# Kernel optimization log

Hardware: AMD Instinct MI355X
Metric: run time of the kernel (lower is better)

The kernel has to match this reference:

```python
import jax, jax.numpy as jnp
import numpy as np
import math

E = 4096  # embed_dim
H = 32    # num_heads
M = 256   # max_queries
B = 8     # batch
N = 256   # kv tokens (16x16 grid -> no pos-embed interpolation branch)


def _sincos_1d(d, pos):
    omega = np.arange(d // 2, dtype=np.float32) / (d / 2.0)
    omega = 1.0 / 10000 ** omega
    out = np.einsum('m,d->md', pos.reshape(-1), omega)
    return np.concatenate([np.sin(out), np.cos(out)], axis=1)


def _sincos_2d(embed_dim, grid_size):
    gh = np.arange(grid_size, dtype=np.float32)
    gw = np.arange(grid_size, dtype=np.float32)
    grid = np.stack(np.meshgrid(gw, gh), axis=0).reshape(2, -1)
    return np.concatenate([
        _sincos_1d(embed_dim // 2, grid[0]),
        _sincos_1d(embed_dim // 2, grid[1]),
    ], axis=1)


def setup_inputs() -> dict:
    key = jax.random.key(0)
    ks = jax.random.split(key, 4)
    grid_size = int(math.ceil(math.sqrt(M)))
    pe = _sincos_2d(E, grid_size)[:M].astype(np.float32)
    return {
        'x': jax.random.normal(ks[0], (B, N, E), jnp.float32),
        'query': 0.02 * jax.random.normal(ks[1], (M, E), jnp.float32),
        'pos_embed': jnp.asarray(pe),
        'ln_q_w': jnp.ones((E,), jnp.float32),
        'ln_q_b': jnp.zeros((E,), jnp.float32),
        'ln_kv_w': jnp.ones((E,), jnp.float32),
        'ln_kv_b': jnp.zeros((E,), jnp.float32),
        'in_proj_w': 0.02 * jax.random.normal(ks[2], (3 * E, E), jnp.float32),
        'in_proj_b': jnp.zeros((3 * E,), jnp.float32),
        'out_proj_w': 0.02 * jax.random.normal(ks[3], (E, E), jnp.float32),
        'out_proj_b': jnp.zeros((E,), jnp.float32),
    }


def _ln(x, w, b, eps=1e-5):
    m = jnp.mean(x, -1, keepdims=True)
    v = jnp.mean((x - m) ** 2, -1, keepdims=True)
    return (x - m) * jax.lax.rsqrt(v + eps) * w + b


def reference(x, query, pos_embed, ln_q_w, ln_q_b, ln_kv_w, ln_kv_b,
              in_proj_w, in_proj_b, out_proj_w, out_proj_b):
    D = E // H
    kv = _ln(x, ln_kv_w, ln_kv_b)                      # [B,N,E] (kv_proj is Identity)
    q_in = _ln(query, ln_q_w, ln_q_b) + pos_embed      # [M,E] (Q + posQ, shared over batch)
    k_in = kv + pos_embed[None]                        # N == M so posK == pos_embed (no interp)
    Wq, Wk, Wv = in_proj_w[:E], in_proj_w[E:2 * E], in_proj_w[2 * E:]
    bq, bk, bv = in_proj_b[:E], in_proj_b[E:2 * E], in_proj_b[2 * E:]
    q = (q_in @ Wq.T + bq).reshape(M, H, D).transpose(1, 0, 2)          # [H,M,D]
    k = (k_in @ Wk.T + bk).reshape(B, N, H, D).transpose(0, 2, 1, 3)    # [B,H,N,D]
    v = (kv @ Wv.T + bv).reshape(B, N, H, D).transpose(0, 2, 1, 3)      # [B,H,N,D]
    scores = jnp.einsum('hmd,bhnd->bhmn', q, k) / jnp.sqrt(jnp.float32(D))
    attn = jax.nn.softmax(scores, axis=-1)                              # [B,H,M,N]
    o = jnp.einsum('bhmn,bhnd->bhmd', attn, v)
    o = o.transpose(0, 2, 1, 3).reshape(B, M, E)
    out = o @ out_proj_w.T + out_proj_b                                 # [B,M,E]
    # need_weights=True with average_attn_weights=True -> head-averaged weights
    return out, attn.mean(axis=1)
```

## Files before the change

kernel.cpp:

```cpp
#include <hip/hip_runtime.h>
#include <hip/hip_bf16.h>

typedef __bf16 bf16;
typedef __attribute__((ext_vector_type(8))) __bf16 bf16x8;
typedef __attribute__((ext_vector_type(4))) __bf16 bf16x4;
typedef __attribute__((ext_vector_type(4))) float floatx4;

#define E_DIM 4096
#define H_DIM 32
#define D_DIM 128
#define M_DIM 256
#define B_DIM 8
#define N_DIM 256

#define GLD_LDS(g, l) __builtin_amdgcn_global_load_lds( \
    (const __attribute__((address_space(1))) unsigned int*)(g), \
    (__attribute__((address_space(3))) unsigned int*)(l), 16, 0, 0)

__device__ __forceinline__ float wave_sum(float v) {
#pragma unroll
  for (int o = 32; o; o >>= 1) v += __shfl_xor(v, o);
  return v;
}
__device__ __forceinline__ float wave_max(float v) {
#pragma unroll
  for (int o = 32; o; o >>= 1) v = fmaxf(v, __shfl_xor(v, o));
  return v;
}

__device__ __forceinline__ void gemm_core(const bf16* __restrict__ Arow,
                                          const bf16* __restrict__ Brow,
                                          int lda, int ldb, int kTiles,
                                          bf16* As, bf16* Bs,
                                          floatx4 (&acc)[4][4],
                                          int wid, int lane) {
  const int s0 = wid * 2;
  const int lp = lane ^ ((lane >> 3) & 7);
  const int srow = lp >> 2;
  const int skoff = (lp & 3) * 8;
  const int rA = (wid >> 1) * 64 + (lane & 15);
  const int rB = (wid & 1) * 64 + (lane & 15);
  const int q16 = (lane >> 4) * 8;
  const int ex = (((lane & 15) >> 1) & 7) << 3;

#pragma unroll
  for (int c = 0; c < 2; ++c) {
    const int s = s0 + c;
    const int row = s * 16 + srow;
    GLD_LDS(Arow + (size_t)row * lda + skoff, As + s * 512);
    GLD_LDS(Brow + (size_t)row * ldb + skoff, Bs + s * 512);
  }

  for (int kt = 0; kt < kTiles; ++kt) {
    const int cur = (kt & 1) * 4096;
    const int nxt = 4096 - cur;
    __syncthreads();
    if (kt + 1 < kTiles) {
      const int k0 = (kt + 1) << 5;
#pragma unroll
      for (int c = 0; c < 2; ++c) {
        const int s = s0 + c;
        const int row = s * 16 + srow;
        GLD_LDS(Arow + (size_t)row * lda + k0 + skoff, As + nxt + s * 512);
        GLD_LDS(Brow + (size_t)row * ldb + k0 + skoff, Bs + nxt + s * 512);
      }
    }
    bf16x8 af[4], bfr[4];
#pragma unroll
    for (int t = 0; t < 4; ++t) {
      af[t] = *(const bf16x8*)(As + cur + ((((rA + t * 16) * 32) + q16) ^ ex));
      bfr[t] = *(const bf16x8*)(Bs + cur + ((((rB + t * 16) * 32) + q16) ^ ex));
    }
#pragma unroll
    for (int tr = 0; tr < 4; ++tr)
#pragma unroll
      for (int tc = 0; tc < 4; ++tc)
        acc[tr][tc] = __builtin_amdgcn_mfma_f32_16x16x32_bf16(af[tr], bfr[tc],
                                                              acc[tr][tc], 0, 0, 0);
  }
}

__global__ __launch_bounds__(256) void cvt_all_kernel(const float* __restrict__ s1,
                                                      bf16* __restrict__ d1,
                                                      const float* __restrict__ s2,
                                                      bf16* __restrict__ d2) {
  long i = ((long)blockIdx.x * 256 + threadIdx.x) * 8;
  const float* src;
  bf16* dst;
  if (i < 50331648L) { src = s1 + i; dst = d1 + i; }
  else { src = s2 + (i - 50331648L); dst = d2 + (i - 50331648L); }
  float4 a = *(const float4*)(src);
  float4 b = *(const float4*)(src + 4);
  bf16x8 p;
  p[0] = (bf16)a.x; p[1] = (bf16)a.y; p[2] = (bf16)a.z; p[3] = (bf16)a.w;
  p[4] = (bf16)b.x; p[5] = (bf16)b.y; p[6] = (bf16)b.z; p[7] = (bf16)b.w;
  *(bf16x8*)(dst) = p;
}

__global__ __launch_bounds__(256) void ln_x_kernel(const float* __restrict__ x,
                                                   const float* __restrict__ w,
                                                   const float* __restrict__ bvec,
                                                   const float* __restrict__ pos,
                                                   bf16* __restrict__ kv,
                                                   bf16* __restrict__ kin) {
  const int row = blockIdx.x;
  const int n = row & (N_DIM - 1);
  const int tid = threadIdx.x, wid = tid >> 6, lane = tid & 63;
  const float* xr = x + (size_t)row * E_DIM;
  float4 v[4];
  float s1 = 0.f, s2 = 0.f;
#pragma unroll
  for (int j = 0; j < 4; ++j) {
    v[j] = *(const float4*)(xr + j * 1024 + tid * 4);
    s1 += v[j].x + v[j].y + v[j].z + v[j].w;
    s2 += v[j].x * v[j].x + v[j].y * v[j].y + v[j].z * v[j].z + v[j].w * v[j].w;
  }
  s1 = wave_sum(s1); s2 = wave_sum(s2);
  __shared__ float red[8];
  if (lane == 0) { red[wid] = s1; red[wid + 4] = s2; }
  __syncthreads();
  s1 = red[0] + red[1] + red[2] + red[3];
  s2 = red[4] + red[5] + red[6] + red[7];
  const float mean = s1 * (1.f / E_DIM);
  const float var = s2 * (1.f / E_DIM) - mean * mean;
  const float rs = rsqrtf(var + 1e-5f);
#pragma unroll
  for (int j = 0; j < 4; ++j) {
    const int idx = j * 1024 + tid * 4;
    float4 wv = *(const float4*)(w + idx);
    float4 bv = *(const float4*)(bvec + idx);
    float4 pv = *(const float4*)(pos + (size_t)n * E_DIM + idx);
    float y0 = (v[j].x - mean) * rs * wv.x + bv.x;
    float y1 = (v[j].y - mean) * rs * wv.y + bv.y;
    float y2 = (v[j].z - mean) * rs * wv.z + bv.z;
    float y3 = (v[j].w - mean) * rs * wv.w + bv.w;
    bf16x4 a; a[0] = (bf16)y0; a[1] = (bf16)y1; a[2] = (bf16)y2; a[3] = (bf16)y3;
    *(bf16x4*)(kv + (size_t)row * E_DIM + idx) = a;
    bf16x4 c; c[0] = (bf16)(y0 + pv.x); c[1] = (bf16)(y1 + pv.y);
    c[2] = (bf16)(y2 + pv.z); c[3] = (bf16)(y3 + pv.w);
    *(bf16x4*)(kin + (size_t)row * E_DIM + idx) = c;
  }
}

__global__ __launch_bounds__(256) void ln_q_kernel(const float* __restrict__ q,
                                                   const float* __restrict__ w,
                                                   const float* __restrict__ bvec,
                                                   const float* __restrict__ pos,
                                                   bf16* __restrict__ qin) {
  const int row = blockIdx.x;
  const int tid = threadIdx.x, wid = tid >> 6, lane = tid & 63;
  const float* xr = q + (size_t)row * E_DIM;
  float4 v[4];
  float s1 = 0.f, s2 = 0.f;
#pragma unroll
  for (int j = 0; j < 4; ++j) {
    v[j] = *(const float4*)(xr + j * 1024 + tid * 4);
    s1 += v[j].x + v[j].y + v[j].z + v[j].w;
    s2 += v[j].x * v[j].x + v[j].y * v[j].y + v[j].z * v[j].z + v[j].w * v[j].w;
  }
  s1 = wave_sum(s1); s2 = wave_sum(s2);
  __shared__ float red[8];
  if (lane == 0) { red[wid] = s1; red[wid + 4] = s2; }
  __syncthreads();
  s1 = red[0] + red[1] + red[2] + red[3];
  s2 = red[4] + red[5] + red[6] + red[7];
  const float mean = s1 * (1.f / E_DIM);
  const float var = s2 * (1.f / E_DIM) - mean * mean;
  const float rs = rsqrtf(var + 1e-5f);
#pragma unroll
  for (int j = 0; j < 4; ++j) {
    const int idx = j * 1024 + tid * 4;
    float4 wv = *(const float4*)(w + idx);
    float4 bv = *(const float4*)(bvec + idx);
    float4 pv = *(const float4*)(pos + (size_t)row * E_DIM + idx);
    bf16x4 a;
    a[0] = (bf16)((v[j].x - mean) * rs * wv.x + bv.x + pv.x);
    a[1] = (bf16)((v[j].y - mean) * rs * wv.y + bv.y + pv.y);
    a[2] = (bf16)((v[j].z - mean) * rs * wv.z + bv.z + pv.z);
    a[3] = (bf16)((v[j].w - mean) * rs * wv.w + bv.w + pv.w);
    *(bf16x4*)(qin + (size_t)row * E_DIM + idx) = a;
  }
}

__global__ __launch_bounds__(256, 4)
void proj_fused(const bf16* __restrict__ qin, const bf16* __restrict__ kin,
                const bf16* __restrict__ kv, const bf16* __restrict__ Wqkv,
                const float* __restrict__ bqkv, bf16* __restrict__ qp,
                bf16* __restrict__ kp, bf16* __restrict__ vt) {
  __shared__ __align__(16) bf16 As[8192];
  __shared__ __align__(16) bf16 Bs[8192];
  const int tid = threadIdx.x;
  const int wid = tid >> 6;
  const int lane = tid & 63;

  const int id = blockIdx.x;
  int role, bx, by;
  const bf16 *A, *B;
  const float* bias;
  bf16* C;
  if (id < 512) {
    role = 1; bx = id & 31; by = id >> 5;
    A = kin; B = Wqkv + 16777216; bias = bqkv + 4096; C = kp;
  } else if (id < 1024) {
    role = 2; bx = (id - 512) & 31; by = (id - 512) >> 5;
    A = kv; B = Wqkv + 33554432; bias = bqkv + 8192; C = vt;
  } else {
    role = 0; bx = (id - 1024) & 31; by = (id - 1024) >> 5;
    A = qin; B = Wqkv; bias = bqkv; C = qp;
  }

  const bf16* Arow = A + (size_t)(by * 128) * E_DIM;
  const bf16* Brow = B + (size_t)(bx * 128) * E_DIM;

  floatx4 acc[4][4];
#pragma unroll
  for (int i = 0; i < 4; ++i)
#pragma unroll
    for (int j = 0; j < 4; ++j) acc[i][j] = (floatx4){0.f, 0.f, 0.f, 0.f};

  gemm_core(Arow, Brow, E_DIM, E_DIM, 128, As, Bs, acc, wid, lane);

  const int mb = by * 128 + (wid >> 1) * 64 + (lane >> 4) * 4;
  const int nb = bx * 128 + (wid & 1) * 64 + (lane & 15);
#pragma unroll
  for (int tr = 0; tr < 4; ++tr) {
#pragma unroll
    for (int tc = 0; tc < 4; ++tc) {
      const int row0 = mb + tr * 16;
      const int col = nb + tc * 16;
      const float bb = bias[col];
      floatx4 a = acc[tr][tc];
      if (role != 2) {
#pragma unroll
        for (int r = 0; r < 4; ++r)
          C[(size_t)(row0 + r) * E_DIM + col] = (bf16)(a[r] + bb);
      } else {
        const int h = col >> 7, d = col & 127;
        const int b_ = row0 >> 8, n_ = row0 & 255;
        bf16x4 p;
#pragma unroll
        for (int r = 0; r < 4; ++r) p[r] = (bf16)(a[r] + bb);
        *(bf16x4*)(C + ((size_t)((b_ * H_DIM + h) * D_DIM + d)) * N_DIM + n_) = p;
      }
    }
  }
}

template <int MODE>
__global__ __launch_bounds__(256, 4)
void gemm_bt(const bf16* __restrict__ Abase, const bf16* __restrict__ Bbase,
             float* __restrict__ Cf, bf16* __restrict__ Cb,
             int K, int lda, int ldb, int ldc, float scale) {
  __shared__ __align__(16) bf16 As[8192];
  __shared__ __align__(16) bf16 Bs[8192];
  const int tid = threadIdx.x;
  const int wid = tid >> 6;
  const int lane = tid & 63;

  const bf16* A = Abase;
  const bf16* B = Bbase;
  if constexpr (MODE == 2) {
    int z = blockIdx.z; int zb = z >> 5, zh = z & 31;
    A += zh * D_DIM;
    B += ((size_t)zb * N_DIM) * E_DIM + zh * D_DIM;
  } else if constexpr (MODE == 3) {
    int z = blockIdx.z;
    A += (size_t)z * M_DIM * 512;
    B += (size_t)z * D_DIM * N_DIM;
  } else if constexpr (MODE == 5) {
    A += blockIdx.z * 2048;
    B += blockIdx.z * 2048;
  }

  const bf16* Arow = A + (size_t)(blockIdx.y * 128) * lda;
  const bf16* Brow = B + (size_t)(blockIdx.x * 128) * ldb;

  floatx4 acc[4][4];
#pragma unroll
  for (int i = 0; i < 4; ++i)
#pragma unroll
    for (int j = 0; j < 4; ++j) acc[i][j] = (floatx4){0.f, 0.f, 0.f, 0.f};

  gemm_core(Arow, Brow, lda, ldb, K >> 5, As, Bs, acc, wid, lane);

  const int mb = blockIdx.y * 128 + (wid >> 1) * 64 + (lane >> 4) * 4;
  const int nb = blockIdx.x * 128 + (wid & 1) * 64 + (lane & 15);
#pragma unroll
  for (int tr = 0; tr < 4; ++tr) {
#pragma unroll
    for (int tc = 0; tc < 4; ++tc) {
      const int row0 = mb + tr * 16;
      const int col = nb + tc * 16;
      floatx4 a = acc[tr][tc];
      if constexpr (MODE == 2) {
#pragma unroll
        for (int r = 0; r < 4; ++r)
          Cf[(size_t)blockIdx.z * (M_DIM * N_DIM) + (size_t)(row0 + r) * ldc + col] =
              a[r] * scale;
      } else if constexpr (MODE == 3) {
        int z = blockIdx.z; int zb_ = z >> 5, zh_ = z & 31;
#pragma unroll
        for (int r = 0; r < 4; ++r)
          Cb[(size_t)zb_ * M_DIM * E_DIM + (size_t)(row0 + r) * E_DIM + zh_ * D_DIM + col] =
              (bf16)a[r];
      } else {
#pragma unroll
        for (int r = 0; r < 4; ++r)
          Cf[(size_t)blockIdx.z * 8388608 + (size_t)(row0 + r) * ldc + col] = a[r];
      }
    }
  }
}

__global__ __launch_bounds__(256) void reduce_out_kernel(const float* __restrict__ p,
                                                         const float* __restrict__ bias,
                                                         float* __restrict__ out) {
  const size_t i = ((size_t)blockIdx.x * 256 + threadIdx.x) * 4;
  float4 a = *(const float4*)(p + i);
  float4 b = *(const float4*)(p + 8388608 + i);
  float4 bb = *(const float4*)(bias + (i & 4095));
  float4 o;
  o.x = a.x + b.x + bb.x; o.y = a.y + b.y + bb.y;
  o.z = a.z + b.z + bb.z; o.w = a.w + b.w + bb.w;
  *(float4*)(out + i) = o;
}

__global__ __launch_bounds__(256) void softmax_mean_kernel(float* __restrict__ scores,
                                                           float* __restrict__ out_mean) {
  const int bm = blockIdx.x;
  const int b = bm >> 8, m = bm & 255;
  const int wid = threadIdx.x >> 6, lane = threadIdx.x & 63;
  float a0 = 0.f, a1 = 0.f, a2 = 0.f, a3 = 0.f;
  for (int j = 0; j < 8; ++j) {
    const int h = wid * 8 + j;
    float* row = scores + ((size_t)((b * H_DIM + h) * M_DIM + m)) * N_DIM;
    float4 v = *(const float4*)(row + lane * 4);
    float mx = fmaxf(fmaxf(v.x, v.y), fmaxf(v.z, v.w));
    mx = wave_max(mx);
    v.x = __expf(v.x - mx); v.y = __expf(v.y - mx);
    v.z = __expf(v.z - mx); v.w = __expf(v.w - mx);
    const float s = wave_sum(v.x + v.y + v.z + v.w);
    const float inv = 1.f / s;
    v.x *= inv; v.y *= inv; v.z *= inv; v.w *= inv;
    a0 += v.x; a1 += v.y; a2 += v.z; a3 += v.w;
    bf16x4 p; p[0] = (bf16)v.x; p[1] = (bf16)v.y; p[2] = (bf16)v.z; p[3] = (bf16)v.w;
    *(bf16x4*)((bf16*)row + lane * 4) = p;
  }
  __shared__ float red[4][256];
  *(float4*)&red[wid][lane * 4] = make_float4(a0, a1, a2, a3);
  __syncthreads();
  if (wid == 0) {
    float4 r0 = *(float4*)&red[0][lane * 4];
    float4 r1 = *(float4*)&red[1][lane * 4];
    float4 r2 = *(float4*)&red[2][lane * 4];
    float4 r3 = *(float4*)&red[3][lane * 4];
    float4 o;
    o.x = (r0.x + r1.x + r2.x + r3.x) * (1.f / H_DIM);
    o.y = (r0.y + r1.y + r2.y + r3.y) * (1.f / H_DIM);
    o.z = (r0.z + r1.z + r2.z + r3.z) * (1.f / H_DIM);
    o.w = (r0.w + r1.w + r2.w + r3.w) * (1.f / H_DIM);
    *(float4*)(out_mean + (size_t)bm * N_DIM + lane * 4) = o;
  }
}

extern "C" void kernel_launch(void* const* d_in, const int* in_sizes, int n_in,
                              void* d_out, int out_size, void* d_ws, size_t ws_size,
                              hipStream_t stream) {
  const float* x = (const float*)d_in[0];
  const float* query = (const float*)d_in[1];
  const float* pos = (const float*)d_in[2];
  const float* ln_q_w = (const float*)d_in[3];
  const float* ln_q_b = (const float*)d_in[4];
  const float* ln_kv_w = (const float*)d_in[5];
  const float* ln_kv_b = (const float*)d_in[6];
  const float* Wqkv_f = (const float*)d_in[7];
  const float* bqkv = (const float*)d_in[8];
  const float* Wout_f = (const float*)d_in[9];
  const float* bout = (const float*)d_in[10];

  char* ws = (char*)d_ws;
  bf16* Wqkv = (bf16*)(ws + 0);
  bf16* Wout = (bf16*)(ws + 100663296);
  bf16* kv   = (bf16*)(ws + 134217728);
  bf16* kin  = (bf16*)(ws + 150994944);
  bf16* qin  = (bf16*)(ws + 167772160);
  bf16* qp   = (bf16*)(ws + 169869312);
  bf16* kp   = (bf16*)(ws + 171966464);
  bf16* vt   = (bf16*)(ws + 188743680);
  float* partials = (float*)(ws + 205520896);
  float* scores = (float*)(ws + 0);
  bf16* obuf = (bf16*)(ws + 67108864);

  float* out = (float*)d_out;
  float* out2 = out + (size_t)B_DIM * M_DIM * E_DIM;

  cvt_all_kernel<<<32768, 256, 0, stream>>>(Wqkv_f, Wqkv, Wout_f, Wout);
  ln_x_kernel<<<2048, 256, 0, stream>>>(x, ln_kv_w, ln_kv_b, pos, kv, kin);
  ln_q_kernel<<<256, 256, 0, stream>>>(query, ln_q_w, ln_q_b, pos, qin);

  proj_fused<<<1088, 256, 0, stream>>>(qin, kin, kv, Wqkv, bqkv, qp, kp, vt);

  gemm_bt<2><<<dim3(2, 2, 256), 256, 0, stream>>>(qp, kp, scores, nullptr,
                                                  128, 4096, 4096, 256,
                                                  0.08838834764831845f);
  softmax_mean_kernel<<<2048, 256, 0, stream>>>(scores, out2);
  gemm_bt<3><<<dim3(1, 2, 256), 256, 0, stream>>>((const bf16*)scores, vt,
                                                  nullptr, obuf,
                                                  256, 512, 256, 4096, 1.f);
  gemm_bt<5><<<dim3(32, 16, 2), 256, 0, stream>>>(obuf, Wout, partials, nullptr,
                                                  2048, 4096, 4096, 4096, 1.f);
  reduce_out_kernel<<<8192, 256, 0, stream>>>(partials, bout, out);
}
```

Baseline: 789.2 us.

## Use 256x256-tile 8-wave pipelined GEMM for QKV and output projections

Replaces the 128x128-tile projection GEMMs with a new 256x256-tile kernel using 512 threads and double-buffered LDS staging via global_load_lds. The main loop interleaves MFMA quarters with async loads, using explicit barriers and setprio. Blocks are remapped in XCD-aware order so the 8 chiplets share the A/B tiles. The larger tiles raise arithmetic intensity and cut global traffic for the two large GEMMs, but give fewer blocks (272 and 256 on 256 CUs) and one block per CU. The small attention GEMMs drop to launch bound 2.

```diff
diff --git a/kernel.cpp b/kernel.cpp
--- a/kernel.cpp
+++ b/kernel.cpp
@@ -28,12 +28,216 @@
   return v;
 }
 
-__device__ __forceinline__ void gemm_core(const bf16* __restrict__ Arow,
-                                          const bf16* __restrict__ Brow,
-                                          int lda, int ldb, int kTiles,
-                                          bf16* As, bf16* Bs,
-                                          floatx4 (&acc)[4][4],
-                                          int wid, int lane) {
+#define BAR256() asm volatile("s_barrier" ::: "memory")
+#define LGKM0_256()                                      \
+  asm volatile("s_waitcnt lgkmcnt(0)" ::: "memory");     \
+  __builtin_amdgcn_sched_barrier(0)
+
+#define STAGE_A256(T, h)                                                       \
+  {                                                                            \
+    _Pragma("unroll") for (int j = 0; j < 2; ++j)                              \
+        GLD_LDS(Ag + (size_t)((h)*128 + sgrow + j * 8) * lda + (T) * 64 + sgcol, \
+                AsP + ((T)&1) * 16384 + (h)*8192 + sdst + j * 512);            \
+  }
+#define STAGE_B256(T, h)                                                       \
+  {                                                                            \
+    _Pragma("unroll") for (int j = 0; j < 2; ++j)                              \
+        GLD_LDS(Bg + (size_t)((h)*128 + sgrow + j * 8) * ldb + (T) * 64 + sgcol, \
+                BsP + ((T)&1) * 16384 + (h)*8192 + sdst + j * 512);            \
+  }
+#define LDA256(mh)                                                             \
+  {                                                                            \
+    _Pragma("unroll") for (int m = 0; m < 4; ++m) {                            \
+      a[m][0] = *(const bf16x8*)(AsP + buf + rA + ((mh)*4 + m) * 1024 + slot0); \
+      a[m][1] = *(const bf16x8*)(AsP + buf + rA + ((mh)*4 + m) * 1024 + slot1); \
+    }                                                                          \
+  }
+#define LDB256(dst, nh)                                                        \
+  {                                                                            \
+    _Pragma("unroll") for (int n = 0; n < 2; ++n) {                            \
+      dst[n][0] = *(const bf16x8*)(BsP + buf + rB + ((nh)*2 + n) * 1024 + slot0); \
+      dst[n][1] = *(const bf16x8*)(BsP + buf + rB + ((nh)*2 + n) * 1024 + slot1); \
+    }                                                                          \
+  }
+#define MFMAQ(mb, nb, B)                                                       \
+  {                                                                            \
+    _Pragma("unroll") for (int m = 0; m < 4; ++m)                              \
+        _Pragma("unroll") for (int n = 0; n < 2; ++n) {                        \
+      acc[(mb) + m][(nb) + n] = __builtin_amdgcn_mfma_f32_16x16x32_bf16(       \
+          a[m][0], B[n][0], acc[(mb) + m][(nb) + n], 0, 0, 0);                 \
+      acc[(mb) + m][(nb) + n] = __builtin_amdgcn_mfma_f32_16x16x32_bf16(       \
+          a[m][1], B[n][1], acc[(mb) + m][(nb) + n], 0, 0, 0);                 \
+    }                                                                          \
+  }
+
+__device__ __forceinline__ void gemm256_core(const bf16* __restrict__ Ag,
+                                             const bf16* __restrict__ Bg,
+                                             int lda, int ldb, int nkt,
+                                             bf16* AsP, bf16* BsP,
+                                             floatx4 (&acc)[8][4],
+                                             int wid, int lane) {
+  const int wm = wid >> 2, wn = wid & 3;
+  const int l15 = lane & 15, q = lane >> 4, e7 = lane & 7;
+  const int slot0 = ((q ^ e7) & 7) * 8;
+  const int slot1 = (((4 + q) ^ e7) & 7) * 8;
+  const int rA = (wm * 128 + l15) * 64;
+  const int rB = (wn * 64 + l15) * 64;
+  const int sgrow = wid * 16 + (lane >> 3);
+  const int sgcol = ((lane & 7) ^ (lane >> 3)) * 8;
+  const int sdst = wid * 1024;
+
+  bf16x8 a[4][2], b0[2][2], b1[2][2];
+
+  STAGE_B256(0, 0); STAGE_B256(0, 1);
+  STAGE_A256(0, 0); STAGE_A256(0, 1);
+  STAGE_B256(1, 0); STAGE_B256(1, 1);
+
+  for (int U = 0; U < nkt; ++U) {
+    const int buf = (U & 1) * 16384;
+    if (U + 1 < nkt)
+      asm volatile("s_waitcnt vmcnt(4)\n\ts_barrier" ::: "memory");
+    else
+      asm volatile("s_waitcnt vmcnt(0)\n\ts_barrier" ::: "memory");
+    LDA256(0); LDB256(b0, 0);
+    if (U + 1 < nkt) { STAGE_A256(U + 1, 0); }
+    BAR256(); LGKM0_256();
+    __builtin_amdgcn_s_setprio(1); MFMAQ(0, 0, b0); __builtin_amdgcn_s_setprio(0);
+    __builtin_amdgcn_sched_barrier(0); BAR256();
+    LDB256(b1, 1);
+    if (U + 1 < nkt) { STAGE_A256(U + 1, 1); }
+    BAR256(); LGKM0_256();
+    __builtin_amdgcn_s_setprio(1); MFMAQ(0, 2, b1); __builtin_amdgcn_s_setprio(0);
+    __builtin_amdgcn_sched_barrier(0); BAR256();
+    LDA256(1);
+    if (U + 2 < nkt) { STAGE_B256(U + 2, 0); }
+    BAR256(); LGKM0_256();
+    __builtin_amdgcn_s_setprio(1); MFMAQ(4, 2, b1); __builtin_amdgcn_s_setprio(0);
+    __builtin_amdgcn_sched_barrier(0); BAR256();
+    if (U + 2 < nkt) { STAGE_B256(U + 2, 1); }
+    BAR256();
+    __builtin_amdgcn_s_setprio(1); MFMAQ(4, 0, b0); __builtin_amdgcn_s_setprio(0);
+    __builtin_amdgcn_sched_barrier(0);
+  }
+}
+
+__global__ __launch_bounds__(512, 1)
+void proj256(const bf16* __restrict__ qin, const bf16* __restrict__ kin,
+             const bf16* __restrict__ kv, const bf16* __restrict__ Wqkv,
+             const float* __restrict__ bqkv, bf16* __restrict__ qp,
+             bf16* __restrict__ kp, bf16* __restrict__ vt) {
+  __shared__ __align__(16) bf16 As2[32768];
+  __shared__ __align__(16) bf16 Bs2[32768];
+  const int tid = threadIdx.x, wid = tid >> 6, lane = tid & 63;
+
+  const int o = blockIdx.x;
+  const int id = (o & 7) * 34 + (o >> 3);
+  int role, bx, by;
+  const bf16 *A, *B;
+  const float* bias;
+  bf16* C;
+  if (id < 128) {
+    role = 1; by = id & 7; bx = id >> 3;
+    A = kin; B = Wqkv + 16777216; bias = bqkv + 4096; C = kp;
+  } else if (id < 256) {
+    role = 2; by = (id - 128) & 7; bx = (id - 128) >> 3;
+    A = kv; B = Wqkv + 33554432; bias = bqkv + 8192; C = vt;
+  } else {
+    role = 0; by = 0; bx = id - 256;
+    A = qin; B = Wqkv; bias = bqkv; C = qp;
+  }
+  const int trowA = by * 256, trowB = bx * 256;
+  const bf16* Ag = A + (size_t)trowA * E_DIM;
+  const bf16* Bg = B + (size_t)trowB * E_DIM;
+
+  floatx4 acc[8][4];
+#pragma unroll
+  for (int i = 0; i < 8; ++i)
+#pragma unroll
+    for (int j = 0; j < 4; ++j) acc[i][j] = (floatx4){0.f, 0.f, 0.f, 0.f};
+
+  gemm256_core(Ag, Bg, E_DIM, E_DIM, 64, As2, Bs2, acc, wid, lane);
+
+  const int wm = wid >> 2, wn = wid & 3;
+  const int l15 = lane & 15, q = lane >> 4;
+  const int mrow0 = trowA + wm * 128 + q * 4;
+  const int ncol0 = trowB + wn * 64 + l15;
+  if (role != 2) {
+#pragma unroll
+    for (int m = 0; m < 8; ++m)
+#pragma unroll
+      for (int n = 0; n < 4; ++n) {
+        const int col = ncol0 + n * 16;
+        const float bb = bias[col];
+        floatx4 v = acc[m][n];
+#pragma unroll
+        for (int r = 0; r < 4; ++r)
+          C[(size_t)(mrow0 + m * 16 + r) * E_DIM + col] = (bf16)(v[r] + bb);
+      }
+  } else {
+#pragma unroll
+    for (int m = 0; m < 8; ++m)
+#pragma unroll
+      for (int n = 0; n < 4; ++n) {
+        const int col = ncol0 + n * 16;
+        const int h = col >> 7, d = col & 127;
+        const float bb = bias[col];
+        const int row0 = mrow0 + m * 16;
+        const int b_ = row0 >> 8, n_ = row0 & 255;
+        floatx4 v = acc[m][n];
+        bf16x4 p;
+#pragma unroll
+        for (int r = 0; r < 4; ++r) p[r] = (bf16)(v[r] + bb);
+        *(bf16x4*)(C + ((size_t)((b_ * H_DIM + h) * D_DIM + d)) * N_DIM + n_) = p;
+      }
+  }
+}
+
+__global__ __launch_bounds__(512, 1)
+void outproj256(const bf16* __restrict__ obuf, const bf16* __restrict__ Wout,
+                float* __restrict__ Cf) {
+  __shared__ __align__(16) bf16 As2[32768];
+  __shared__ __align__(16) bf16 Bs2[32768];
+  const int tid = threadIdx.x, wid = tid >> 6, lane = tid & 63;
+
+  const int o = blockIdx.x;
+  const int id = (o & 7) * 32 + (o >> 3);
+  const int z = id >> 7;
+  const int t = id & 127;
+  const int by = t & 7, bx = t >> 3;
+  const int trowA = by * 256, trowB = bx * 256;
+  const bf16* Ag = obuf + (size_t)z * 2048 + (size_t)trowA * E_DIM;
+  const bf16* Bg = Wout + (size_t)z * 2048 + (size_t)trowB * E_DIM;
+
+  floatx4 acc[8][4];
+#pragma unroll
+  for (int i = 0; i < 8; ++i)
+#pragma unroll
+    for (int j = 0; j < 4; ++j) acc[i][j] = (floatx4){0.f, 0.f, 0.f, 0.f};
+
+  gemm256_core(Ag, Bg, E_DIM, E_DIM, 32, As2, Bs2, acc, wid, lane);
+
+  const int wm = wid >> 2, wn = wid & 3;
+  const int l15 = lane & 15, q = lane >> 4;
+  const int mrow0 = trowA + wm * 128 + q * 4;
+  const int ncol0 = trowB + wn * 64 + l15;
+#pragma unroll
+  for (int m = 0; m < 8; ++m)
+#pragma unroll
+    for (int n = 0; n < 4; ++n) {
+      const int col = ncol0 + n * 16;
+      floatx4 v = acc[m][n];
+#pragma unroll
+      for (int r = 0; r < 4; ++r)
+        Cf[(size_t)z * 8388608 + (size_t)(mrow0 + m * 16 + r) * E_DIM + col] = v[r];
+    }
+}
+
+__device__ __forceinline__ void gemm_core_small(const bf16* __restrict__ Arow,
+                                                const bf16* __restrict__ Brow,
+                                                int lda, int ldb, int kTiles,
+                                                bf16* As, bf16* Bs,
+                                                floatx4 (&acc)[4][4],
+                                                int wid, int lane) {
   const int s0 = wid * 2;
   const int lp = lane ^ ((lane >> 3) & 7);
   const int srow = lp >> 2;
@@ -182,72 +386,8 @@
   }
 }
 
-__global__ __launch_bounds__(256, 4)
-void proj_fused(const bf16* __restrict__ qin, const bf16* __restrict__ kin,
-                const bf16* __restrict__ kv, const bf16* __restrict__ Wqkv,
-                const float* __restrict__ bqkv, bf16* __restrict__ qp,
-                bf16* __restrict__ kp, bf16* __restrict__ vt) {
-  __shared__ __align__(16) bf16 As[8192];
-  __shared__ __align__(16) bf16 Bs[8192];
-  const int tid = threadIdx.x;
-  const int wid = tid >> 6;
-  const int lane = tid & 63;
-
-  const int id = blockIdx.x;
-  int role, bx, by;
-  const bf16 *A, *B;
-  const float* bias;
-  bf16* C;
-  if (id < 512) {
-    role = 1; bx = id & 31; by = id >> 5;
-    A = kin; B = Wqkv + 16777216; bias = bqkv + 4096; C = kp;
-  } else if (id < 1024) {
-    role = 2; bx = (id - 512) & 31; by = (id - 512) >> 5;
-    A = kv; B = Wqkv + 33554432; bias = bqkv + 8192; C = vt;
-  } else {
-    role = 0; bx = (id - 1024) & 31; by = (id - 1024) >> 5;
-    A = qin; B = Wqkv; bias = bqkv; C = qp;
-  }
-
-  const bf16* Arow = A + (size_t)(by * 128) * E_DIM;
-  const bf16* Brow = B + (size_t)(bx * 128) * E_DIM;
-
-  floatx4 acc[4][4];
-#pragma unroll
-  for (int i = 0; i < 4; ++i)
-#pragma unroll
-    for (int j = 0; j < 4; ++j) acc[i][j] = (floatx4){0.f, 0.f, 0.f, 0.f};
-
-  gemm_core(Arow, Brow, E_DIM, E_DIM, 128, As, Bs, acc, wid, lane);
-
-  const int mb = by * 128 + (wid >> 1) * 64 + (lane >> 4) * 4;
-  const int nb = bx * 128 + (wid & 1) * 64 + (lane & 15);
-#pragma unroll
-  for (int tr = 0; tr < 4; ++tr) {
-#pragma unroll
-    for (int tc = 0; tc < 4; ++tc) {
-      const int row0 = mb + tr * 16;
-      const int col = nb + tc * 16;
-      const float bb = bias[col];
-      floatx4 a = acc[tr][tc];
-      if (role != 2) {
-#pragma unroll
-        for (int r = 0; r < 4; ++r)
-          C[(size_t)(row0 + r) * E_DIM + col] = (bf16)(a[r] + bb);
-      } else {
-        const int h = col >> 7, d = col & 127;
-        const int b_ = row0 >> 8, n_ = row0 & 255;
-        bf16x4 p;
-#pragma unroll
-        for (int r = 0; r < 4; ++r) p[r] = (bf16)(a[r] + bb);
-        *(bf16x4*)(C + ((size_t)((b_ * H_DIM + h) * D_DIM + d)) * N_DIM + n_) = p;
-      }
-    }
-  }
-}
-
 template <int MODE>
-__global__ __launch_bounds__(256, 4)
+__global__ __launch_bounds__(256, 2)
 void gemm_bt(const bf16* __restrict__ Abase, const bf16* __restrict__ Bbase,
              float* __restrict__ Cf, bf16* __restrict__ Cb,
              int K, int lda, int ldb, int ldc, float scale) {
@@ -267,9 +407,6 @@
     int z = blockIdx.z;
     A += (size_t)z * M_DIM * 512;
     B += (size_t)z * D_DIM * N_DIM;
-  } else if constexpr (MODE == 5) {
-    A += blockIdx.z * 2048;
-    B += blockIdx.z * 2048;
   }
 
   const bf16* Arow = A + (size_t)(blockIdx.y * 128) * lda;
@@ -281,7 +418,7 @@
 #pragma unroll
     for (int j = 0; j < 4; ++j) acc[i][j] = (floatx4){0.f, 0.f, 0.f, 0.f};
 
-  gemm_core(Arow, Brow, lda, ldb, K >> 5, As, Bs, acc, wid, lane);
+  gemm_core_small(Arow, Brow, lda, ldb, K >> 5, As, Bs, acc, wid, lane);
 
   const int mb = blockIdx.y * 128 + (wid >> 1) * 64 + (lane >> 4) * 4;
   const int nb = blockIdx.x * 128 + (wid & 1) * 64 + (lane & 15);
@@ -297,16 +434,12 @@
         for (int r = 0; r < 4; ++r)
           Cf[(size_t)blockIdx.z * (M_DIM * N_DIM) + (size_t)(row0 + r) * ldc + col] =
               a[r] * scale;
-      } else if constexpr (MODE == 3) {
+      } else {
         int z = blockIdx.z; int zb_ = z >> 5, zh_ = z & 31;
 #pragma unroll
         for (int r = 0; r < 4; ++r)
           Cb[(size_t)zb_ * M_DIM * E_DIM + (size_t)(row0 + r) * E_DIM + zh_ * D_DIM + col] =
               (bf16)a[r];
-      } else {
-#pragma unroll
-        for (int r = 0; r < 4; ++r)
-          Cf[(size_t)blockIdx.z * 8388608 + (size_t)(row0 + r) * ldc + col] = a[r];
       }
     }
   }
@@ -398,7 +531,7 @@
   ln_x_kernel<<<2048, 256, 0, stream>>>(x, ln_kv_w, ln_kv_b, pos, kv, kin);
   ln_q_kernel<<<256, 256, 0, stream>>>(query, ln_q_w, ln_q_b, pos, qin);
 
-  proj_fused<<<1088, 256, 0, stream>>>(qin, kin, kv, Wqkv, bqkv, qp, kp, vt);
+  proj256<<<272, 512, 0, stream>>>(qin, kin, kv, Wqkv, bqkv, qp, kp, vt);
 
   gemm_bt<2><<<dim3(2, 2, 256), 256, 0, stream>>>(qp, kp, scores, nullptr,
                                                   128, 4096, 4096, 256,
@@ -407,7 +540,6 @@
   gemm_bt<3><<<dim3(1, 2, 256), 256, 0, stream>>>((const bf16*)scores, vt,
                                                   nullptr, obuf,
                                                   256, 512, 256, 4096, 1.f);
-  gemm_bt<5><<<dim3(32, 16, 2), 256, 0, stream>>>(obuf, Wout, partials, nullptr,
-                                                  2048, 4096, 4096, 4096, 1.f);
+  outproj256<<<256, 512, 0, stream>>>(obuf, Wout, partials);
   reduce_out_kernel<<<8192, 256, 0, stream>>>(partials, bout, out);
 }
```

New measurement: 827.6 us. +4.9%, slower.
